# Kernel tuning notes

Hardware: AMD Instinct MI355X
Metric: run time of the kernel (lower is better)

Reference implementation:

```python
import jax, jax.numpy as jnp
import numpy as np

K = 51  # separable kernel taps
PAD = (K - 1) // 2  # 25


def _lerp_axis(a, n_in, n_out, axis):
    # 1D bilinear resample with align_corners=True semantics
    pos = jnp.arange(n_out, dtype=jnp.float32) * (float(n_in - 1) / float(n_out - 1))
    lo = jnp.floor(pos).astype(jnp.int32)
    hi = jnp.minimum(lo + 1, n_in - 1)
    w = (pos - lo.astype(jnp.float32)).astype(a.dtype)
    shp = [1] * a.ndim
    shp[axis] = n_out
    w = w.reshape(shp)
    return jnp.take(a, lo, axis=axis) * (1 - w) + jnp.take(a, hi, axis=axis) * w


def upsample2x_align_corners(x):
    B, C, H, W = x.shape
    x = _lerp_axis(x, H, 2 * H, 2)
    x = _lerp_axis(x, W, 2 * W, 3)
    return x


def conv3x3(x, w, b):
    y = jax.lax.conv_general_dilated(
        x, w, window_strides=(1, 1), padding=((1, 1), (1, 1)),
        dimension_numbers=('NCHW', 'OIHW', 'NCHW'))
    return y + b[None, :, None, None]


def kernel_block(x, w1, b1, w2, b2, w3, b3):
    h = upsample2x_align_corners(x)
    h = jax.nn.relu(conv3x3(h, w1, b1))
    h = jax.nn.relu(conv3x3(h, w2, b2))
    h = jax.nn.relu(conv3x3(h, w3, b3))
    return h  # [B, 51, H, W]


def sep_conv(img, kv, kh):
    # img: [B,C,H+K-1,W+K-1]; kv, kh: [B,K,H,W]
    # out[b,c,y,x] = sum_{i,j} img[b,c,y+i,x+j] * kv[b,i,y,x] * kh[b,j,y,x]
    B, C, Hp, Wp = img.shape
    H, W = kv.shape[2], kv.shape[3]
    # vertical sliding windows: [B,C,K,H,Wp]
    vwin = jnp.stack([img[:, :, i:i + H, :] for i in range(K)], axis=2)
    out = jnp.zeros((B, C, H, W), img.dtype)
    for j in range(K):  # static loop over K taps
        t = jnp.einsum('bciyx,biyx->bcyx', vwin[:, :, :, :, j:j + W], kv)
        out = out + t * kh[:, j][:, None]
    return out


def setup_inputs() -> dict:
    key = jax.random.key(0)
    ks = jax.random.split(key, 9)
    B, Cf, Hh, Wh = 4, 64, 128, 128  # feature map (half res)
    H, W = 2 * Hh, 2 * Wh
    x = jax.random.normal(ks[0], (B, Cf, Hh, Wh), jnp.float32)
    i1 = jax.random.normal(ks[1], (B, 3, H + 2 * PAD, W + 2 * PAD), jnp.float32)
    i2 = jax.random.normal(ks[2], (B, 3, H + 2 * PAD, W + 2 * PAD), jnp.float32)
    s = 0.05
    W1 = jax.random.normal(ks[3], (4, K, Cf, 3, 3), jnp.float32) * s
    B1 = jax.random.normal(ks[4], (4, K), jnp.float32) * s
    W2 = jax.random.normal(ks[5], (4, K, K, 3, 3), jnp.float32) * s
    B2 = jax.random.normal(ks[6], (4, K), jnp.float32) * s
    W3 = jax.random.normal(ks[7], (4, K, K, 3, 3), jnp.float32) * s
    B3 = jax.random.normal(ks[8], (4, K), jnp.float32) * s
    return {'x': x, 'i1': i1, 'i2': i2,
            'W1': W1, 'B1': B1, 'W2': W2, 'B2': B2, 'W3': W3, 'B3': B3}


def reference(x, i1, i2, W1, B1, W2, B2, W3, B3):
    kernels = [kernel_block(x, W1[k], B1[k], W2[k], B2[k], W3[k], B3[k])
               for k in range(4)]
    k1v, k1h, k2v, k2h = kernels
    y = sep_conv(i1, k1v, k1h) + sep_conv(i2, k2v, k2h)
    return y
```

## Files before the change

### kernel.cpp

```cpp
#include <hip/hip_runtime.h>
#include <stdint.h>

#define HH 128
#define H 256
#define W 256
#define KK 51
#define HIMG 306
#define WIMG 306
#define CF 64
#define BB 4
#define HWN (H * W)
#define CHAIN ((size_t)HWN * 64)

typedef short bhalf8 __attribute__((ext_vector_type(8)));
typedef float f32x4 __attribute__((ext_vector_type(4)));

__device__ inline uint16_t f2bf(float f) {
    uint32_t u = __builtin_bit_cast(uint32_t, f);
    u += 0x7FFF + ((u >> 16) & 1);
    return (uint16_t)(u >> 16);
}
__device__ inline float bf2f(uint16_t h) {
    uint32_t u = ((uint32_t)h) << 16;
    return __builtin_bit_cast(float, u);
}
__device__ inline bhalf8 aload(const uint16_t* wp, int k, int tap, int m, int chf, int lane) {
    return *(const bhalf8*)(wp + ((((size_t)(k * 9 + tap) * 4 + m) * 2 + chf) * 64 + lane) * 8);
}
__device__ inline void gload_lds16(const void* g, void* l) {
    __builtin_amdgcn_global_load_lds(
        (const __attribute__((address_space(1))) unsigned int*)g,
        (__attribute__((address_space(3))) unsigned int*)l, 16, 0, 0);
}

__global__ __launch_bounds__(256) void upsample_cvt(const float* __restrict__ xin,
                                                    uint16_t* __restrict__ upT) {
    const int z = blockIdx.z;
    xin += (size_t)z * CF * HH * HH;
    upT += (size_t)z * CHAIN;
    __shared__ float SU[2][64][19];
    const int y = blockIdx.x, x0 = blockIdx.y * 32;
    const float s = 127.f / 255.f;
    float py = y * s; int ly = (int)py; int hy = min(ly + 1, 127); float wy = py - (float)ly;
    int lx0 = (int)(x0 * s);
    for (int t = threadIdx.x; t < 2 * 64 * 18; t += 256) {
        int col = t % 18; int c = (t / 18) & 63; int row = t / (18 * 64);
        int sy = row ? hy : ly;
        int sx = min(lx0 + col, 127);
        SU[row][c][col] = xin[((size_t)c * 128 + sy) * 128 + sx];
    }
    __syncthreads();
    const int xl = threadIdx.x & 31, cg = threadIdx.x >> 5;
    const int x = x0 + xl;
    float px = x * s; int lx = (int)px; float wx = px - (float)lx;
    int lxl = lx - lx0;
    int hxl = min(lx + 1, 127) - lx0;
    uint32_t d[4];
#pragma unroll
    for (int q4 = 0; q4 < 4; ++q4) {
        uint32_t two[2];
#pragma unroll
        for (int e = 0; e < 2; ++e) {
            int c = cg * 8 + q4 * 2 + e;
            float v00 = SU[0][c][lxl], v01 = SU[0][c][hxl];
            float v10 = SU[1][c][lxl], v11 = SU[1][c][hxl];
            float a = v00 * (1.f - wy) + v10 * wy;
            float b = v01 * (1.f - wy) + v11 * wy;
            two[e] = f2bf(a * (1.f - wx) + b * wx);
        }
        d[q4] = two[0] | (two[1] << 16);
    }
    uint4 v = {d[0], d[1], d[2], d[3]};
    *(uint4*)(upT + ((size_t)y * W + x) * 64 + cg * 8) = v;
}

__global__ void wprep(const float* __restrict__ wsrc, uint16_t* __restrict__ wdst, int cin_act) {
    int g = blockIdx.x * 256 + threadIdx.x;
    if (g >= 4 * 9 * 4 * 2 * 64) return;
    int lane = g & 63;
    int q = g >> 6;
    int ch = q & 1; q >>= 1;
    int m = q & 3; q >>= 2;
    int tap = q % 9;
    int k = q / 9;
    int co = m * 16 + (lane & 15);
    int ci0 = ch * 32 + (lane >> 4) * 8;
    uint32_t d[4];
#pragma unroll
    for (int p = 0; p < 4; ++p) {
        uint32_t w2[2];
#pragma unroll
        for (int e = 0; e < 2; ++e) {
            int ci = ci0 + p * 2 + e;
            float v = 0.f;
            if (co < KK && ci < cin_act)
                v = wsrc[((size_t)(k * KK + co) * cin_act + ci) * 9 + tap];
            w2[e] = f2bf(v);
        }
        d[p] = w2[0] | (w2[1] << 16);
    }
    uint4 v = {d[0], d[1], d[2], d[3]};
    *(uint4*)(wdst + (size_t)g * 8) = v;
}

__global__ __launch_bounds__(512, 4)
void conv_mfma(const uint16_t* __restrict__ in, const uint16_t* __restrict__ wp,
               const float* __restrict__ bias, uint16_t* __restrict__ out,
               size_t in_cstride, size_t in_bstride, int kbase) {
    const int wg = blockIdx.x;
    const int id = (wg & 7) * ((int)gridDim.x >> 3) + (wg >> 3);
    const int z = id >> 8;
    const int rem = id & 255;
    const int y0 = (rem & 63) * 4;
    const int x0 = (rem >> 6) * 64;

    const int k = kbase + (z & 3);
    in  += (size_t)(z & 3) * in_cstride + (size_t)(z >> 2) * in_bstride;
    out += (size_t)z * CHAIN;
    const int tid = threadIdx.x;
    const int lane = tid & 63;
    const int wv = tid >> 6;
    const int l4 = lane & 15, g = lane >> 4;

    __shared__ uint4 lds[6 * 66 * 8];

    unsigned oobmask = 0;
#pragma unroll
    for (int it = 0; it < 7; ++it) {
        int t = tid + it * 512;
        if (t < 6 * 66 * 8) {
            int c = t & 7;
            int q = t >> 3;
            int xl = q % 66;
            int r = q / 66;
            int yg = y0 - 1 + r;
            int xg = x0 + xl - 1;
            if ((unsigned)yg >= H || (unsigned)xg >= W) {
                oobmask |= 1u << it;
                yg = min(max(yg, 0), H - 1);
                xg = min(max(xg, 0), W - 1);
            }
            int cs = c ^ (xl & 7);
            gload_lds16(in + (((size_t)yg * W + xg) * 64 + cs * 8),
                        (char*)lds + ((size_t)it * 512 + wv * 64) * 16);
        }
    }
    asm volatile("s_waitcnt vmcnt(0)" ::: "memory");
#pragma unroll
    for (int it = 0; it < 7; ++it) {
        int t = tid + it * 512;
        if ((oobmask & (1u << it)) && t < 6 * 66 * 8)
            lds[t] = (uint4){0u, 0u, 0u, 0u};
    }
    __syncthreads();

    const int row = wv & 3;
    const int nh = (wv >> 2) * 2;
    const int y = y0 + row;

    f32x4 acc[4][2];
#pragma unroll
    for (int m = 0; m < 4; ++m)
#pragma unroll
        for (int nn = 0; nn < 2; ++nn)
            acc[m][nn] = (f32x4){0.f, 0.f, 0.f, 0.f};

    __builtin_amdgcn_s_setprio(1);
#pragma unroll
    for (int chf = 0; chf < 2; ++chf) {
#pragma unroll
        for (int tap = 0; tap < 9; ++tap) {
            const int ky = tap / 3, kx = tap % 3;
            bhalf8 afr[4];
#pragma unroll
            for (int m = 0; m < 4; ++m) afr[m] = aload(wp, k, tap, m, chf, lane);
            const int rrow = row + ky;
#pragma unroll
            for (int nn = 0; nn < 2; ++nn) {
                int xl = (nh + nn) * 16 + l4 + kx;
                int slot = (chf * 4 + g) ^ (xl & 7);
                bhalf8 bfr = *(const bhalf8*)&lds[((size_t)rrow * 66 + xl) * 8 + slot];
#pragma unroll
                for (int m = 0; m < 4; ++m)
                    acc[m][nn] = __builtin_amdgcn_mfma_f32_16x16x32_bf16(afr[m], bfr, acc[m][nn], 0, 0, 0);
            }
        }
    }
    __builtin_amdgcn_s_setprio(0);

    __syncthreads();
    ushort* ST = (ushort*)lds + wv * 2048;
#pragma unroll
    for (int m = 0; m < 4; ++m) {
        int co0 = m * 16 + g * 4;
        float bvr[4];
#pragma unroll
        for (int r = 0; r < 4; ++r)
            bvr[r] = (co0 + r < KK) ? bias[k * KK + co0 + r] : 0.f;
#pragma unroll
        for (int nn = 0; nn < 2; ++nn) {
            int pxl = nn * 16 + l4;
            uint32_t pk[2];
#pragma unroll
            for (int hh = 0; hh < 2; ++hh) {
                uint32_t lo = f2bf(fmaxf(acc[m][nn][hh * 2]     + bvr[hh * 2],     0.f));
                uint32_t hi = f2bf(fmaxf(acc[m][nn][hh * 2 + 1] + bvr[hh * 2 + 1], 0.f));
                pk[hh] = lo | (hi << 16);
            }
            int idx = pxl * 64 + (co0 ^ ((pxl & 7) << 3));
            *(uint2*)(ST + idx) = (uint2){pk[0], pk[1]};
        }
    }
    const int p8 = lane >> 3;
    const int ch = lane & 7;
#pragma unroll
    for (int it = 0; it < 4; ++it) {
        int px = it * 8 + p8;
        uint4 v = *(const uint4*)(ST + px * 64 + ((ch ^ (px & 7)) << 3));
        *(uint4*)(out + (((size_t)y * W + x0 + nh * 16 + px) * 64 + ch * 8)) = v;
    }
}

__global__ __launch_bounds__(256, 2)
void sepconv3(const float* __restrict__ img,
              const uint16_t* __restrict__ kvT, const uint16_t* __restrict__ khT,
              float* __restrict__ out, int accum) {
    __shared__ uint4 SB[320 * 8];
    __shared__ float SC[4][16 * 83];
    const int y = blockIdx.x, c = blockIdx.y, z = blockIdx.z;
    const int tid = threadIdx.x, lane = tid & 63, wv = tid >> 6;
    const float* ip = img + (size_t)(z * 3 + c) * HIMG * WIMG;
    kvT += (size_t)z * 4 * CHAIN;
    khT += (size_t)z * 4 * CHAIN;

    for (int task = tid; task < 40 * 64; task += 256) {
        int i = task & 63;
        int u0 = (task >> 6) * 8;
        float f[8];
        bool rowok = (i <= 50);
        const float* rp = ip + (size_t)(y + i) * WIMG;
#pragma unroll
        for (int e2 = 0; e2 < 4; ++e2) {
            int u = u0 + e2 * 2;
            float2 v2 = (rowok && u < WIMG) ? *(const float2*)(rp + u) : float2{0.f, 0.f};
            f[e2 * 2] = v2.x; f[e2 * 2 + 1] = v2.y;
        }
#pragma unroll
        for (int e = 0; e < 8; ++e) {
            int u = u0 + e;
            *((ushort*)SB + u * 64 + (((i >> 3) ^ (u & 7)) << 3) + (i & 7)) = f2bf(f[e]);
        }
    }
    __syncthreads();

    const int l4 = lane & 15, g = lane >> 4;
    for (int xt = 0; xt < 4; ++xt) {
        const int x0 = (wv * 4 + xt) * 16;
        const int xpix = x0 + l4;
        bhalf8 a0 = *(const bhalf8*)(kvT + ((size_t)y * W + xpix) * 64 + g * 8);
        bhalf8 a1 = *(const bhalf8*)(kvT + ((size_t)y * W + xpix) * 64 + 32 + g * 8);
        f32x4 acc[5];
#pragma unroll
        for (int nt = 0; nt < 5; ++nt) acc[nt] = (f32x4){0.f, 0.f, 0.f, 0.f};
#pragma unroll
        for (int nt = 0; nt < 5; ++nt) {
            int u = x0 + nt * 16 + l4;
            bhalf8 b0 = *(const bhalf8*)((ushort*)SB + u * 64 + ((g ^ (u & 7)) << 3));
            acc[nt] = __builtin_amdgcn_mfma_f32_16x16x32_bf16(a0, b0, acc[nt], 0, 0, 0);
            bhalf8 b1 = *(const bhalf8*)((ushort*)SB + u * 64 + (((4 + g) ^ (u & 7)) << 3));
            acc[nt] = __builtin_amdgcn_mfma_f32_16x16x32_bf16(a1, b1, acc[nt], 0, 0, 0);
        }
#pragma unroll
        for (int nt = 0; nt < 5; ++nt)
#pragma unroll
            for (int r = 0; r < 4; ++r)
                SC[wv][(g * 4 + r) * 83 + nt * 16 + l4] = acc[nt][r];

        const uint16_t* khp = khT + ((size_t)y * W + xpix) * 64;
        float partial = 0.f;
#pragma unroll
        for (int jj = 0; jj < 13; ++jj) {
            int j = g * 13 + jj;
            if (j < KK)
                partial = fmaf(SC[wv][l4 * 83 + l4 + j], bf2f(khp[j]), partial);
        }
        partial += __shfl_xor(partial, 16);
        partial += __shfl_xor(partial, 32);
        if (g == 0) {
            size_t oi = ((size_t)(z * 3 + c) * H + y) * W + xpix;
            if (accum) out[oi] += partial;
            else       out[oi] = partial;
        }
    }
}

extern "C" void kernel_launch(void* const* d_in, const int* in_sizes, int n_in,
                              void* d_out, int out_size, void* d_ws, size_t ws_size,
                              hipStream_t stream) {
    const float* x  = (const float*)d_in[0];
    const float* i1 = (const float*)d_in[1];
    const float* i2 = (const float*)d_in[2];
    const float* W1 = (const float*)d_in[3];
    const float* B1 = (const float*)d_in[4];
    const float* W2 = (const float*)d_in[5];
    const float* B2 = (const float*)d_in[6];
    const float* W3 = (const float*)d_in[7];
    const float* B3 = (const float*)d_in[8];
    float* out = (float*)d_out;

    char* wsb = (char*)d_ws;
    const size_t IMGB = CHAIN * 2;
    const size_t WPN  = 4 * 9 * 4 * 2 * 64 * 8;

    uint16_t* wp1 = (uint16_t*)d_out;
    uint16_t* wp2 = wp1 + WPN;
    uint16_t* wp3 = wp2 + WPN;
    wprep<<<72, 256, 0, stream>>>(W1, wp1, CF);
    wprep<<<72, 256, 0, stream>>>(W2, wp2, KK);
    wprep<<<72, 256, 0, stream>>>(W3, wp3, KK);

    if (ws_size >= 32 * IMGB) {
        uint16_t* A   = (uint16_t*)wsb;
        uint16_t* Bb  = (uint16_t*)(wsb + 16 * IMGB);
        uint16_t* upT = Bb + 12 * CHAIN;

        upsample_cvt<<<dim3(H, 8, BB), 256, 0, stream>>>(x, upT);
        conv_mfma<<<dim3(64 * 4 * 16), 512, 0, stream>>>(upT, wp1, B1, A, 0, CHAIN, 0);
        conv_mfma<<<dim3(64 * 4 * 16), 512, 0, stream>>>(A,  wp2, B2, Bb, CHAIN, 4 * CHAIN, 0);
        conv_mfma<<<dim3(64 * 4 * 16), 512, 0, stream>>>(Bb, wp3, B3, A,  CHAIN, 4 * CHAIN, 0);
        sepconv3<<<dim3(H, 3, BB), 256, 0, stream>>>(i1, A,             A + CHAIN,     out, 0);
        sepconv3<<<dim3(H, 3, BB), 256, 0, stream>>>(i2, A + 2 * CHAIN, A + 3 * CHAIN, out, 1);
    } else if (ws_size >= 13 * IMGB) {
        uint16_t* r1  = (uint16_t*)wsb;
        uint16_t* r2  = (uint16_t*)(wsb + 4 * IMGB);
        uint16_t* r3  = (uint16_t*)(wsb + 8 * IMGB);
        uint16_t* upT = (uint16_t*)(wsb + 12 * IMGB);
        for (int b = 0; b < BB; ++b) {
            upsample_cvt<<<dim3(H, 8, 1), 256, 0, stream>>>(x + (size_t)b * CF * HH * HH, upT);
            conv_mfma<<<dim3(64 * 4 * 4), 512, 0, stream>>>(upT, wp1, B1, r1, 0, 0, 0);
            conv_mfma<<<dim3(64 * 4 * 4), 512, 0, stream>>>(r1, wp2, B2, r2, CHAIN, 0, 0);
            conv_mfma<<<dim3(64 * 4 * 4), 512, 0, stream>>>(r2, wp3, B3, r3, CHAIN, 0, 0);
            for (int p = 0; p < 2; ++p) {
                const float* img = (p ? i2 : i1) + (size_t)b * 3 * HIMG * WIMG;
                sepconv3<<<dim3(H, 3, 1), 256, 0, stream>>>(img,
                        r3 + (size_t)(2 * p) * CHAIN, r3 + (size_t)(2 * p + 1) * CHAIN,
                        out + (size_t)b * 3 * HWN, p);
            }
        }
    } else {
        uint16_t* upT = (uint16_t*)wsb;
        uint16_t* t1  = (uint16_t*)(wsb + 1 * IMGB);
        uint16_t* t2  = (uint16_t*)(wsb + 3 * IMGB);
        uint16_t* t3  = (uint16_t*)(wsb + 5 * IMGB);
        for (int b = 0; b < BB; ++b) {
            upsample_cvt<<<dim3(H, 8, 1), 256, 0, stream>>>(x + (size_t)b * CF * HH * HH, upT);
            for (int p = 0; p < 2; ++p) {
                conv_mfma<<<dim3(64 * 4 * 2), 512, 0, stream>>>(upT, wp1, B1, t1, 0, 0, 2 * p);
                conv_mfma<<<dim3(64 * 4 * 2), 512, 0, stream>>>(t1, wp2, B2, t2, CHAIN, 0, 2 * p);
                conv_mfma<<<dim3(64 * 4 * 2), 512, 0, stream>>>(t2, wp3, B3, t3, CHAIN, 0, 2 * p);
                const float* img = (p ? i2 : i1) + (size_t)b * 3 * HIMG * WIMG;
                sepconv3<<<dim3(H, 3, 1), 256, 0, stream>>>(img, t3, t3 + CHAIN,
                        out + (size_t)b * 3 * HWN, p);
            }
        }
    }
}
```

Before: 513.6 us.

## Split conv halo load into two channel halves to overlap loads with MFMA

The conv kernel's LDS halo tile is split into two channel-half buffers, each with its own XOR swizzle. Compute on the first half starts after a partial vmcnt wait, and the second half's loads finish while the first half's MFMAs run. Launch bounds drop from 4 to 3 blocks per SM, and the prepared weights move to the end of the output buffer. The extra barrier and the lower occupancy hint could offset the gain from the overlap.

```diff
diff --git a/kernel.cpp b/kernel.cpp
--- a/kernel.cpp
+++ b/kernel.cpp
@@ -11,6 +11,7 @@
 #define BB 4
 #define HWN (H * W)
 #define CHAIN ((size_t)HWN * 64)
+#define HALFCH 1584
 
 typedef short bhalf8 __attribute__((ext_vector_type(8)));
 typedef float f32x4 __attribute__((ext_vector_type(4)));
@@ -103,7 +104,7 @@
     *(uint4*)(wdst + (size_t)g * 8) = v;
 }
 
-__global__ __launch_bounds__(512, 4)
+__global__ __launch_bounds__(512, 3)
 void conv_mfma(const uint16_t* __restrict__ in, const uint16_t* __restrict__ wp,
                const float* __restrict__ bias, uint16_t* __restrict__ out,
                size_t in_cstride, size_t in_bstride, int kbase) {
@@ -122,35 +123,45 @@
     const int wv = tid >> 6;
     const int l4 = lane & 15, g = lane >> 4;
 
-    __shared__ uint4 lds[6 * 66 * 8];
-
-    unsigned oobmask = 0;
-#pragma unroll
-    for (int it = 0; it < 7; ++it) {
-        int t = tid + it * 512;
-        if (t < 6 * 66 * 8) {
-            int c = t & 7;
-            int q = t >> 3;
-            int xl = q % 66;
-            int r = q / 66;
-            int yg = y0 - 1 + r;
-            int xg = x0 + xl - 1;
-            if ((unsigned)yg >= H || (unsigned)xg >= W) {
-                oobmask |= 1u << it;
-                yg = min(max(yg, 0), H - 1);
-                xg = min(max(xg, 0), W - 1);
-            }
-            int cs = c ^ (xl & 7);
-            gload_lds16(in + (((size_t)yg * W + xg) * 64 + cs * 8),
-                        (char*)lds + ((size_t)it * 512 + wv * 64) * 16);
-        }
-    }
-    asm volatile("s_waitcnt vmcnt(0)" ::: "memory");
-#pragma unroll
-    for (int it = 0; it < 7; ++it) {
-        int t = tid + it * 512;
-        if ((oobmask & (1u << it)) && t < 6 * 66 * 8)
-            lds[t] = (uint4){0u, 0u, 0u, 0u};
+    __shared__ uint4 lds[2 * HALFCH];
+
+    unsigned oob0 = 0, oob1 = 0;
+#pragma unroll
+    for (int hf = 0; hf < 2; ++hf) {
+#pragma unroll
+        for (int it = 0; it < 4; ++it) {
+            int i = it * 512 + tid;
+            if (i < HALFCH) {
+                int c4 = i & 3;
+                int q = i >> 2;
+                int xl = q % 66;
+                int r = q / 66;
+                int yg = y0 - 1 + r;
+                int xg = x0 + xl - 1;
+                if ((unsigned)yg >= H || (unsigned)xg >= W) {
+                    if (hf == 0) oob0 |= 1u << it; else oob1 |= 1u << it;
+                    yg = min(max(yg, 0), H - 1);
+                    xg = min(max(xg, 0), W - 1);
+                }
+                int cs = hf * 4 + (c4 ^ (xl & 3));
+                gload_lds16(in + (((size_t)yg * W + xg) * 64 + cs * 8),
+                            (char*)lds + ((size_t)hf * HALFCH + i) * 16);
+            }
+        }
+    }
+
+    f32x4 acc[4][2];
+#pragma unroll
+    for (int m = 0; m < 4; ++m)
+#pragma unroll
+        for (int nn = 0; nn < 2; ++nn)
+            acc[m][nn] = (f32x4){0.f, 0.f, 0.f, 0.f};
+
+    asm volatile("s_waitcnt vmcnt(3)" ::: "memory");
+#pragma unroll
+    for (int it = 0; it < 4; ++it) {
+        int i = it * 512 + tid;
+        if ((oob0 & (1u << it)) && i < HALFCH) lds[i] = (uint4){0u, 0u, 0u, 0u};
     }
     __syncthreads();
 
@@ -158,16 +169,19 @@
     const int nh = (wv >> 2) * 2;
     const int y = y0 + row;
 
-    f32x4 acc[4][2];
-#pragma unroll
-    for (int m = 0; m < 4; ++m)
-#pragma unroll
-        for (int nn = 0; nn < 2; ++nn)
-            acc[m][nn] = (f32x4){0.f, 0.f, 0.f, 0.f};
-
-    __builtin_amdgcn_s_setprio(1);
 #pragma unroll
     for (int chf = 0; chf < 2; ++chf) {
+        if (chf) {
+            asm volatile("s_waitcnt vmcnt(0)" ::: "memory");
+#pragma unroll
+            for (int it = 0; it < 4; ++it) {
+                int i = it * 512 + tid;
+                if ((oob1 & (1u << it)) && i < HALFCH)
+                    lds[HALFCH + i] = (uint4){0u, 0u, 0u, 0u};
+            }
+            __syncthreads();
+        }
+        __builtin_amdgcn_s_setprio(1);
 #pragma unroll
         for (int tap = 0; tap < 9; ++tap) {
             const int ky = tap / 3, kx = tap % 3;
@@ -178,15 +192,16 @@
 #pragma unroll
             for (int nn = 0; nn < 2; ++nn) {
                 int xl = (nh + nn) * 16 + l4 + kx;
-                int slot = (chf * 4 + g) ^ (xl & 7);
-                bhalf8 bfr = *(const bhalf8*)&lds[((size_t)rrow * 66 + xl) * 8 + slot];
+                int slot = g ^ (xl & 3);
+                bhalf8 bfr = *(const bhalf8*)&lds[(size_t)chf * HALFCH
+                                                  + ((size_t)rrow * 66 + xl) * 4 + slot];
 #pragma unroll
                 for (int m = 0; m < 4; ++m)
                     acc[m][nn] = __builtin_amdgcn_mfma_f32_16x16x32_bf16(afr[m], bfr, acc[m][nn], 0, 0, 0);
             }
         }
-    }
-    __builtin_amdgcn_s_setprio(0);
+        __builtin_amdgcn_s_setprio(0);
+    }
 
     __syncthreads();
     ushort* ST = (ushort*)lds + wv * 2048;
@@ -312,7 +327,7 @@
     const size_t IMGB = CHAIN * 2;
     const size_t WPN  = 4 * 9 * 4 * 2 * 64 * 8;
 
-    uint16_t* wp1 = (uint16_t*)d_out;
+    uint16_t* wp1 = (uint16_t*)((char*)d_out + (size_t)out_size * 4 - 3 * WPN * 2);
     uint16_t* wp2 = wp1 + WPN;
     uint16_t* wp3 = wp2 + WPN;
     wprep<<<72, 256, 0, stream>>>(W1, wp1, CF);
```

New measurement: 535.1 us. +4.2%, slower.
